# Kernel optimization log

Hardware: AMD Instinct MI355X
Metric: run time of the kernel (lower is better)

Reference implementation:

```python
import jax, jax.numpy as jnp
import numpy as np

B, S, E = 4, 2048, 512
H, D = 8, 64
MIN_W, MAX_W = 256, 1024
EPS = 1e-6


def setup_inputs() -> dict:
    key = jax.random.key(0)
    ks = jax.random.split(key, 9)
    w = lambda k, shp: jax.random.normal(k, shp, dtype=jnp.float32) * 0.02
    return {
        "x": jax.random.normal(ks[0], (B, S, E), dtype=jnp.float32),
        "rms1_w": jnp.ones((E,), jnp.float32),
        "rms2_w": jnp.ones((E,), jnp.float32),
        "qkv_w": w(ks[1], (3 * E, E)),
        "out_w": w(ks[2], (E, E)),
        "cs_w1": w(ks[3], (E // 4, E)),
        "cs_w2": w(ks[4], (1, E // 4)),
        "gate_w": w(ks[5], (2304, E)),
        "up_w": w(ks[6], (2304, E)),
        "down_w": w(ks[7], (E, 2304)),
    }


def _rmsnorm(x, w):
    rms = jax.lax.rsqrt(jnp.mean(x * x, axis=-1, keepdims=True) + EPS)
    return x * rms * w


def _rotate_half(x):
    x1 = x[..., ::2]
    x2 = x[..., 1::2]
    return jnp.stack((-x2, x1), axis=-1).reshape(x.shape)


def reference(x, rms1_w, rms2_w, qkv_w, out_w, cs_w1, cs_w2, gate_w, up_w, down_w):
    # --- pre-norm ---
    h = _rmsnorm(x, rms1_w)                                  # [B,S,E]
    # --- qkv ---
    qkv = h @ qkv_w.T                                        # [B,S,3E]
    qkv = qkv.reshape(B, S, 3, H, D).transpose(2, 0, 3, 1, 4)
    q, k, v = qkv[0], qkv[1], qkv[2]                         # [B,H,S,D]
    # --- RoPE (cat-freqs cos/sin + interleaved rotate_half, as in source) ---
    inv_freq = 1.0 / (10000.0 ** (jnp.arange(0, D, 2, dtype=jnp.float32) / D))
    pos = jnp.arange(S, dtype=jnp.float32)
    freqs = jnp.outer(pos, inv_freq)                         # [S,D/2]
    emb = jnp.concatenate([freqs, freqs], axis=-1)           # [S,D]
    cos = jnp.cos(emb)[None, None]
    sin = jnp.sin(emb)[None, None]
    q = q * cos + _rotate_half(q) * sin
    k = k * cos + _rotate_half(k) * sin
    # --- attention scores ---
    scale = D ** -0.5
    scores = jnp.einsum("bhqd,bhkd->bhqk", q, k) * scale     # [B,H,S,S]
    # --- complexity -> dynamic window size ---
    n = S * E
    mu = jnp.mean(h, axis=(1, 2), keepdims=True)
    var = jnp.sum((h - mu) ** 2, axis=(1, 2)) / (n - 1)      # unbiased, per batch
    var_norm = jax.nn.sigmoid(var * 10.0 - 5.0)
    xm = jnp.mean(h, axis=1)                                 # [B,E]
    learned = jax.nn.sigmoid((jax.nn.silu(xm @ cs_w1.T)) @ cs_w2.T)[:, 0]
    complexity = (var_norm + learned) / 2.0                  # [B]
    ws_f = MIN_W + jnp.mean(complexity) * (MAX_W - MIN_W)
    ws = ws_f.astype(jnp.int32)                              # trunc, like .int()
    ws = jnp.maximum(jnp.minimum(ws, S), MIN_W)
    # --- causal + sliding-window mask ---
    p = jnp.arange(S)
    rel = p[:, None] - p[None, :]                            # [S,S]
    allowed = (rel >= 0) & (rel < ws)
    scores = jnp.where(allowed[None, None], scores, -jnp.inf)
    attn = jax.nn.softmax(scores, axis=-1)
    out = jnp.einsum("bhqk,bhkd->bhqd", attn, v)             # [B,H,S,D]
    out = out.transpose(0, 2, 1, 3).reshape(B, S, E)
    out = out @ out_w.T
    x = x + out
    # --- SwiGLU FFN ---
    h2 = _rmsnorm(x, rms2_w)
    ffn = (jax.nn.silu(h2 @ gate_w.T) * (h2 @ up_w.T)) @ down_w.T
    return x + ffn
```

## Files before the change

kernel.cpp:

```cpp
#include <hip/hip_runtime.h>

typedef unsigned short u16;
typedef unsigned int   u32;
typedef __attribute__((ext_vector_type(4))) float  f32x4;
typedef __attribute__((ext_vector_type(8))) __bf16 bf16x8;
typedef __attribute__((ext_vector_type(4))) u32    u32x4;
typedef __attribute__((ext_vector_type(2))) u32    u32x2;

#define B_ 4
#define S_ 2048
#define E_ 512
#define H_ 8
#define D_ 64

__device__ __forceinline__ u16 f2bf(float f) {
  union { float f; u32 u; } a; a.f = f;
  u32 r = a.u + 0x7FFFu + ((a.u >> 16) & 1u);
  return (u16)(r >> 16);
}
__device__ __forceinline__ float bf2f(u16 u) {
  union { u32 u; float f; } a; a.u = (u32)u << 16;
  return a.f;
}
__device__ __forceinline__ u32 pkbf(float lo, float hi) {
  u32 r;
  asm("v_cvt_pk_bf16_f32 %0, %1, %2" : "=v"(r) : "v"(lo), "v"(hi));
  return r;
}

#define GLOAD16(gp, lp) __builtin_amdgcn_global_load_lds( \
    (const __attribute__((address_space(1))) void*)(gp),  \
    (__attribute__((address_space(3))) void*)(lp), 16, 0, 0)

__global__ __launch_bounds__(256) void cvt_k(const float* __restrict__ s,
                                             u16* __restrict__ d, int n) {
  int i = (blockIdx.x * 256 + threadIdx.x) * 4;
  if (i >= n) return;
  f32x4 v = *(const f32x4*)(s + i);
  u32x2 o;
  o.x = pkbf(v[0], v[1]);
  o.y = pkbf(v[2], v[3]);
  *(u32x2*)(d + i) = o;
}

__global__ __launch_bounds__(256) void ropetab_k(float* __restrict__ ct,
                                                 float* __restrict__ st) {
  int idx = blockIdx.x * 256 + threadIdx.x;
  int s = idx >> 6, j = idx & 63;
  float f = powf(10000.f, -(float)(j & 31) * (1.f / 32.f));
  float ang = (float)s * f;
  ct[idx] = cosf(ang);
  st[idx] = sinf(ang);
}

__global__ __launch_bounds__(256) void rmsnorm_k(const float* __restrict__ x,
                                                 const float* __restrict__ wv,
                                                 u16* __restrict__ o) {
  const int row = blockIdx.x;
  const int t = threadIdx.x;
  const float* xr = x + (size_t)row * E_;
  float v0 = xr[t], v1 = xr[t + 256];
  float ss = v0 * v0 + v1 * v1;
#pragma unroll
  for (int m = 1; m < 64; m <<= 1) ss += __shfl_xor(ss, m, 64);
  __shared__ float red[4];
  if ((t & 63) == 0) red[t >> 6] = ss;
  __syncthreads();
  float tot = red[0] + red[1] + red[2] + red[3];
  float rms = 1.f / sqrtf(tot * (1.f / (float)E_) + 1e-6f);
  o[(size_t)row * E_ + t]       = f2bf(v0 * rms * wv[t]);
  o[(size_t)row * E_ + t + 256] = f2bf(v1 * rms * wv[t + 256]);
}

__global__ __launch_bounds__(256) void colsum_k(const u16* __restrict__ h,
                                                float* __restrict__ st) {
  const int b = blockIdx.x >> 3, ck = blockIdx.x & 7;
  const u16* hb = h + ((size_t)b * S_ + ck * 256) * E_;
  const int t = threadIdx.x;
  float a0 = 0, a1 = 0, s = 0, sq = 0;
  for (int r = 0; r < 256; ++r) {
    float v0 = bf2f(hb[(size_t)r * E_ + t]);
    float v1 = bf2f(hb[(size_t)r * E_ + t + 256]);
    a0 += v0; a1 += v1;
    s += v0 + v1; sq += v0 * v0 + v1 * v1;
  }
  atomicAdd(&st[8 + b * E_ + t], a0);
  atomicAdd(&st[8 + b * E_ + t + 256], a1);
#pragma unroll
  for (int m = 1; m < 64; m <<= 1) { s += __shfl_xor(s, m, 64); sq += __shfl_xor(sq, m, 64); }
  if ((t & 63) == 0) { atomicAdd(&st[b], s); atomicAdd(&st[4 + b], sq); }
}

__global__ __launch_bounds__(128) void wscalc_k(float* __restrict__ st,
                                                const float* __restrict__ w1,
                                                const float* __restrict__ w2) {
  const int j = threadIdx.x;
  __shared__ float comp[4];
  __shared__ float tw[2];
  float dot[4] = {0.f, 0.f, 0.f, 0.f};
  const float* w1r = w1 + (size_t)j * E_;
  for (int e = 0; e < E_; ++e) {
    float wv = w1r[e];
    dot[0] += st[8 + 0 * E_ + e] * wv;
    dot[1] += st[8 + 1 * E_ + e] * wv;
    dot[2] += st[8 + 2 * E_ + e] * wv;
    dot[3] += st[8 + 3 * E_ + e] * wv;
  }
  for (int b = 0; b < 4; ++b) {
    float d = dot[b] * (1.f / (float)S_);
    float si = d / (1.f + __expf(-d));
    float term = si * w2[j];
#pragma unroll
    for (int m = 1; m < 64; m <<= 1) term += __shfl_xor(term, m, 64);
    __syncthreads();
    if ((j & 63) == 0) tw[j >> 6] = term;
    __syncthreads();
    if (j == 0) {
      float pre = tw[0] + tw[1];
      float learned = 1.f / (1.f + __expf(-pre));
      const float n = (float)S_ * (float)E_;
      float sum = st[b], ssq = st[4 + b];
      float var = (ssq - sum * sum / n) / (n - 1.f);
      float vn = 1.f / (1.f + __expf(-(var * 10.f - 5.f)));
      comp[b] = 0.5f * (vn + learned);
    }
    __syncthreads();
  }
  if (j == 0) {
    float mean = 0.25f * (comp[0] + comp[1] + comp[2] + comp[3]);
    float wsf = 256.f + mean * 768.f;
    int v = (int)wsf;
    v = v < 256 ? 256 : (v > S_ ? S_ : v);
    ((int*)st)[2056] = v;
  }
}

struct EpiArgs {
  u16* q; u16* k; u16* vt;
  const float* cosT; const float* sinT;
  const float* resid; float* outf;
};

template <int N, int K, int EPI, int WAVES>
__global__ __launch_bounds__(WAVES * 64) void gemm_k(const u16* __restrict__ A,
                                                     const u16* __restrict__ W,
                                                     EpiArgs ea) {
  __shared__ u16 sA[128 * 32];
  __shared__ u16 sB[128 * 32];
  const int tid = threadIdx.x;
  const int bm = blockIdx.x, bn = blockIdx.y;
  const int lane = tid & 63, w = tid >> 6;
  const int g = lane >> 4, c = lane & 15;
  constexpr int MI = (WAVES == 4) ? 4 : 2;
  const int wrow = (w >> 1) * ((WAVES == 4) ? 64 : 32);
  const int wcol = (w & 1) * 64;

  const int srow = tid >> 2, sch = tid & 3;
  const u16* gA = A + (size_t)(bm * 128 + srow) * K + sch * 8;
  const u16* gB = W + (size_t)(bn * 128 + srow) * K + sch * 8;
  char* lA0 = (char*)sA + w * 1024;
  char* lB0 = (char*)sB + w * 1024;

  f32x4 acc[MI][4];
  f32x4 zz = {0.f, 0.f, 0.f, 0.f};
#pragma unroll
  for (int i = 0; i < MI; ++i)
#pragma unroll
    for (int j = 0; j < 4; ++j) acc[i][j] = zz;

  for (int it = 0; it < K / 32; ++it) {
    const int ko = it * 32;
    GLOAD16(gA + ko, lA0);
    GLOAD16(gB + ko, lB0);
    if constexpr (WAVES == 4) {
      GLOAD16(gA + (size_t)64 * K + ko, lA0 + 4096);
      GLOAD16(gB + (size_t)64 * K + ko, lB0 + 4096);
    }
    __syncthreads();
    bf16x8 af[MI], bfr[4];
#pragma unroll
    for (int mi = 0; mi < MI; ++mi)
      af[mi] = *(const bf16x8*)&sA[(wrow + mi * 16 + c) * 32 + g * 8];
#pragma unroll
    for (int nj = 0; nj < 4; ++nj)
      bfr[nj] = *(const bf16x8*)&sB[(wcol + nj * 16 + c) * 32 + g * 8];
#pragma unroll
    for (int mi = 0; mi < MI; ++mi)
#pragma unroll
      for (int nj = 0; nj < 4; ++nj)
        acc[mi][nj] = __builtin_amdgcn_mfma_f32_16x16x32_bf16(af[mi], bfr[nj], acc[mi][nj], 0, 0, 0);
    __syncthreads();
  }

#pragma unroll
  for (int mi = 0; mi < MI; ++mi) {
#pragma unroll
    for (int nj = 0; nj < 4; ++nj) {
      const int rowb = bm * 128 + wrow + mi * 16 + 4 * g;
      const int cc = bn * 128 + wcol + nj * 16 + c;
      if constexpr (EPI == 0) {
        const int which = cc >> 9;
        const int hh = (cc >> 6) & 7;
        const int d = cc & 63;
        const int bi = rowb >> 11;
        const int s = rowb & (S_ - 1);
        if (which == 2) {
          u32x2 pk;
          pk.x = pkbf(acc[mi][nj][0], acc[mi][nj][1]);
          pk.y = pkbf(acc[mi][nj][2], acc[mi][nj][3]);
          *(u32x2*)(ea.vt + (((size_t)(bi * H_ + hh) * D_ + d) * S_ + s)) = pk;
        } else {
          u16* dst = (which == 0 ? ea.q : ea.k) + (((size_t)(bi * H_ + hh) * S_ + s) * D_ + d);
#pragma unroll
          for (int r = 0; r < 4; ++r) {
            float v = acc[mi][nj][r];
            float pv = __shfl_xor(v, 1, 64);
            int si = s + r;
            float cs = ea.cosT[si * 64 + d];
            float sn = ea.sinT[si * 64 + d];
            float o = v * cs + ((d & 1) ? pv : -pv) * sn;
            dst[(size_t)r * D_] = f2bf(o);
          }
        }
      } else {
#pragma unroll
        for (int r = 0; r < 4; ++r) {
          size_t idx = (size_t)(rowb + r) * N + cc;
          ea.outf[idx] = acc[mi][nj][r] + ea.resid[idx];
        }
      }
    }
  }
}

__global__ __launch_bounds__(512) void gemmgu_k(const u16* __restrict__ A,
                                                const u16* __restrict__ Wg,
                                                const u16* __restrict__ Wu,
                                                u16* __restrict__ outb) {
  __shared__ u16 sA[128 * 32];
  __shared__ u16 sG[128 * 32];
  __shared__ u16 sU[128 * 32];
  const int tid = threadIdx.x;
  const int bm = blockIdx.x, bn = blockIdx.y;
  const int lane = tid & 63, w = tid >> 6;
  const int g = lane >> 4, c = lane & 15;
  const int wrow = (w >> 1) * 32;
  const int wcol = (w & 1) * 64;

  const int srow = tid >> 2, sch = tid & 3;
  const u16* gA = A + (size_t)(bm * 128 + srow) * 512 + sch * 8;
  const u16* gG = Wg + (size_t)(bn * 128 + srow) * 512 + sch * 8;
  const u16* gU = Wu + (size_t)(bn * 128 + srow) * 512 + sch * 8;
  char* lA0 = (char*)sA + w * 1024;
  char* lG0 = (char*)sG + w * 1024;
  char* lU0 = (char*)sU + w * 1024;

  f32x4 accg[2][4], accu[2][4];
  f32x4 zz = {0.f, 0.f, 0.f, 0.f};
#pragma unroll
  for (int i = 0; i < 2; ++i)
#pragma unroll
    for (int j = 0; j < 4; ++j) { accg[i][j] = zz; accu[i][j] = zz; }

  for (int it = 0; it < 16; ++it) {
    const int ko = it * 32;
    GLOAD16(gA + ko, lA0);
    GLOAD16(gG + ko, lG0);
    GLOAD16(gU + ko, lU0);
    __syncthreads();
    bf16x8 af[2], bg[4], bu[4];
#pragma unroll
    for (int mi = 0; mi < 2; ++mi)
      af[mi] = *(const bf16x8*)&sA[(wrow + mi * 16 + c) * 32 + g * 8];
#pragma unroll
    for (int nj = 0; nj < 4; ++nj) {
      bg[nj] = *(const bf16x8*)&sG[(wcol + nj * 16 + c) * 32 + g * 8];
      bu[nj] = *(const bf16x8*)&sU[(wcol + nj * 16 + c) * 32 + g * 8];
    }
#pragma unroll
    for (int mi = 0; mi < 2; ++mi)
#pragma unroll
      for (int nj = 0; nj < 4; ++nj) {
        accg[mi][nj] = __builtin_amdgcn_mfma_f32_16x16x32_bf16(af[mi], bg[nj], accg[mi][nj], 0, 0, 0);
        accu[mi][nj] = __builtin_amdgcn_mfma_f32_16x16x32_bf16(af[mi], bu[nj], accu[mi][nj], 0, 0, 0);
      }
    __syncthreads();
  }

#pragma unroll
  for (int mi = 0; mi < 2; ++mi) {
#pragma unroll
    for (int nj = 0; nj < 4; ++nj) {
      const int rowb = bm * 128 + wrow + mi * 16 + 4 * g;
      const int cc = bn * 128 + wcol + nj * 16 + c;
#pragma unroll
      for (int r = 0; r < 4; ++r) {
        float gv = accg[mi][nj][r];
        float uv = accu[mi][nj][r];
        float sil = gv / (1.f + __expf(-gv));
        outb[(size_t)(rowb + r) * 2304 + cc] = f2bf(sil * uv);
      }
    }
  }
}

__global__ __launch_bounds__(256) void attn_k(const u16* __restrict__ Qb,
                                              const u16* __restrict__ Kb,
                                              const u16* __restrict__ Vt,
                                              u16* __restrict__ ao,
                                              const int* __restrict__ wsp) {
  const int bh = blockIdx.x;
  const int b = bh >> 3, h = bh & 7;
  const int qt = blockIdx.y;
  const int tid = threadIdx.x;
  const int w = tid >> 6, lane = tid & 63;
  const int g = lane >> 4, c = lane & 15;
  const int ws = *wsp;
  const int qw = qt * 64 + w * 16;
  const u16* Qh = Qb + (size_t)bh * S_ * D_;
  const u16* Kh = Kb + (size_t)bh * S_ * D_;
  const u16* Vh = Vt + (size_t)bh * D_ * S_;

  bf16x8 qf0 = *(const bf16x8*)(Qh + (qw + c) * D_ + g * 8);
  bf16x8 qf1 = *(const bf16x8*)(Qh + (qw + c) * D_ + 32 + g * 8);

  const float SCL = 0.125f * 1.44269504089f;
  float m2 = -3e38f, lsum = 0.f;
  f32x4 O[4];
  f32x4 zz = {0.f, 0.f, 0.f, 0.f};
#pragma unroll
  for (int i = 0; i < 4; ++i) O[i] = zz;

  int lo = qw - ws + 1;
  if (lo < 0) lo = 0;
  const int q = qw + c;
  for (int kb = lo & ~63; kb <= qw + 15; kb += 64) {
    f32x4 st[4];
#pragma unroll
    for (int t = 0; t < 4; ++t) {
      const u16* kp = Kh + (kb + 16 * t + c) * D_;
      f32x4 s = zz;
      s = __builtin_amdgcn_mfma_f32_16x16x32_bf16(*(const bf16x8*)(kp + g * 8), qf0, s, 0, 0, 0);
      s = __builtin_amdgcn_mfma_f32_16x16x32_bf16(*(const bf16x8*)(kp + 32 + g * 8), qf1, s, 0, 0, 0);
      st[t] = s;
    }
    float p[4][4];
    float bm = -3e38f;
#pragma unroll
    for (int t = 0; t < 4; ++t)
#pragma unroll
      for (int r = 0; r < 4; ++r) {
        int ki = kb + 16 * t + 4 * g + r;
        float v = st[t][r] * SCL;
        bool ok = (q >= ki) && (q - ki) < ws;
        p[t][r] = ok ? v : -__builtin_inff();
        bm = fmaxf(bm, p[t][r]);
      }
    bm = fmaxf(bm, __shfl_xor(bm, 16, 64));
    bm = fmaxf(bm, __shfl_xor(bm, 32, 64));
    if (!__all(bm - m2 <= 8.f)) {
      float mnew = fmaxf(m2, bm);
      float al = exp2f(m2 - mnew);
      lsum *= al;
#pragma unroll
      for (int i = 0; i < 4; ++i) O[i] *= al;
      m2 = mnew;
    }
    float psum = 0.f;
#pragma unroll
    for (int t = 0; t < 4; ++t)
#pragma unroll
      for (int r = 0; r < 4; ++r) {
        p[t][r] = exp2f(p[t][r] - m2);
        psum += p[t][r];
      }
    psum += __shfl_xor(psum, 16, 64);
    psum += __shfl_xor(psum, 32, 64);
    lsum += psum;

    u32 pp[4][2];
#pragma unroll
    for (int t = 0; t < 4; ++t) {
      pp[t][0] = pkbf(p[t][0], p[t][1]);
      pp[t][1] = pkbf(p[t][2], p[t][3]);
    }
    const int lA = (g & 1) * 32 + c;
    const int lB = lA + 16;
    const int hi = g >> 1;
    union { bf16x8 v; u32 u[4]; } pf0, pf1;
#pragma unroll
    for (int wi = 0; wi < 2; ++wi) {
      u32 a0 = (u32)__shfl((int)pp[0][wi], lA, 64);
      u32 a1 = (u32)__shfl((int)pp[1][wi], lA, 64);
      u32 a2 = (u32)__shfl((int)pp[2][wi], lA, 64);
      u32 a3 = (u32)__shfl((int)pp[3][wi], lA, 64);
      u32 b0 = (u32)__shfl((int)pp[0][wi], lB, 64);
      u32 b1 = (u32)__shfl((int)pp[1][wi], lB, 64);
      u32 b2 = (u32)__shfl((int)pp[2][wi], lB, 64);
      u32 b3 = (u32)__shfl((int)pp[3][wi], lB, 64);
      pf0.u[wi]     = hi ? a1 : a0;
      pf0.u[2 + wi] = hi ? b1 : b0;
      pf1.u[wi]     = hi ? a3 : a2;
      pf1.u[2 + wi] = hi ? b3 : b2;
    }
#pragma unroll
    for (int dt = 0; dt < 4; ++dt) {
      const u16* vp = Vh + (size_t)(dt * 16 + c) * S_ + kb;
      O[dt] = __builtin_amdgcn_mfma_f32_16x16x32_bf16(*(const bf16x8*)(vp + g * 8), pf0.v, O[dt], 0, 0, 0);
      O[dt] = __builtin_amdgcn_mfma_f32_16x16x32_bf16(*(const bf16x8*)(vp + 32 + g * 8), pf1.v, O[dt], 0, 0, 0);
    }
  }

  float inv = 1.f / lsum;
  __shared__ u16 ob[4][16][80];
#pragma unroll
  for (int dt = 0; dt < 4; ++dt)
#pragma unroll
    for (int r = 0; r < 4; ++r)
      ob[w][c][dt * 16 + 4 * g + r] = f2bf(O[dt][r] * inv);
  __syncthreads();
#pragma unroll
  for (int it = 0; it < 2; ++it) {
    int linear = tid + it * 256;
    int qrow = linear >> 3, ch = linear & 7;
    u32x4 v = *(const u32x4*)&ob[qrow >> 4][qrow & 15][ch * 8];
    *(u32x4*)(ao + ((size_t)(b * S_ + qt * 64 + qrow)) * E_ + h * D_ + ch * 8) = v;
  }
}

extern "C" void kernel_launch(void* const* d_in, const int* in_sizes, int n_in,
                              void* d_out, int out_size, void* d_ws, size_t ws_size,
                              hipStream_t stream) {
  const float* x      = (const float*)d_in[0];
  const float* rms1_w = (const float*)d_in[1];
  const float* rms2_w = (const float*)d_in[2];
  const float* qkv_w  = (const float*)d_in[3];
  const float* out_w  = (const float*)d_in[4];
  const float* cs_w1  = (const float*)d_in[5];
  const float* cs_w2  = (const float*)d_in[6];
  const float* gate_w = (const float*)d_in[7];
  const float* up_w   = (const float*)d_in[8];
  const float* down_w = (const float*)d_in[9];

  char* ws = (char*)d_ws;
  constexpr size_t o_wqkv = 0;
  constexpr size_t o_wout = 1572864;
  constexpr size_t o_wgate = 2097152;
  constexpr size_t o_wup = 4456448;
  constexpr size_t o_wdown = 6815744;
  constexpr size_t o_h = 9175040;
  constexpr size_t o_stats = 17563648;
  constexpr size_t o_cos = 17580032;
  constexpr size_t o_sin = 18104320;
  constexpr size_t o_Q = 18628608;
  constexpr size_t o_K = 27017216;
  constexpr size_t o_Vt = 35405824;
  constexpr size_t o_x2 = 43794432;
  constexpr size_t o_gate = 60571648;

  u16* wqkv = (u16*)(ws + o_wqkv);
  u16* wout = (u16*)(ws + o_wout);
  u16* wgate = (u16*)(ws + o_wgate);
  u16* wup = (u16*)(ws + o_wup);
  u16* wdown = (u16*)(ws + o_wdown);
  u16* h = (u16*)(ws + o_h);
  float* stats = (float*)(ws + o_stats);
  float* cosT = (float*)(ws + o_cos);
  float* sinT = (float*)(ws + o_sin);
  u16* Qb = (u16*)(ws + o_Q);
  u16* Kb = (u16*)(ws + o_K);
  u16* Vt = (u16*)(ws + o_Vt);
  float* x2 = (float*)(ws + o_x2);
  u16* gateb = (u16*)(ws + o_gate);
  u16* attno = h;
  u16* h2 = Qb;

  hipMemsetAsync(stats, 0, 16384, stream);
  cvt_k<<<768, 256, 0, stream>>>(qkv_w, wqkv, 1536 * 512);
  cvt_k<<<256, 256, 0, stream>>>(out_w, wout, 512 * 512);
  cvt_k<<<1152, 256, 0, stream>>>(gate_w, wgate, 2304 * 512);
  cvt_k<<<1152, 256, 0, stream>>>(up_w, wup, 2304 * 512);
  cvt_k<<<1152, 256, 0, stream>>>(down_w, wdown, 512 * 2304);
  ropetab_k<<<512, 256, 0, stream>>>(cosT, sinT);

  rmsnorm_k<<<8192, 256, 0, stream>>>(x, rms1_w, h);
  colsum_k<<<32, 256, 0, stream>>>(h, stats);
  wscalc_k<<<1, 128, 0, stream>>>(stats, cs_w1, cs_w2);

  EpiArgs ea{};
  ea.q = Qb; ea.k = Kb; ea.vt = Vt; ea.cosT = cosT; ea.sinT = sinT;
  gemm_k<1536, 512, 0, 4><<<dim3(64, 12), 256, 0, stream>>>(h, wqkv, ea);

  attn_k<<<dim3(32, 32), 256, 0, stream>>>(Qb, Kb, Vt, attno, (const int*)(stats + 2056));

  EpiArgs e2{};
  e2.resid = x; e2.outf = x2;
  gemm_k<512, 512, 1, 8><<<dim3(64, 4), 512, 0, stream>>>(attno, wout, e2);

  rmsnorm_k<<<8192, 256, 0, stream>>>(x2, rms2_w, h2);

  gemmgu_k<<<dim3(64, 18), 512, 0, stream>>>(h2, wgate, wup, gateb);

  EpiArgs e5{};
  e5.resid = x2; e5.outf = (float*)d_out;
  gemm_k<512, 2304, 1, 8><<<dim3(64, 4), 512, 0, stream>>>(gateb, wdown, e5);

  (void)in_sizes; (void)n_in; (void)out_size; (void)ws_size;
}
```

Baseline: 402.8 us.

## Double-buffer GEMM LDS, swizzle block order, and hoist K/V loads in attention

The GEMM kernels now use two LDS buffers, so the next K-slice is loaded while MFMAs run on the current one, which drops one barrier per iteration. Block IDs move to a flattened grid, remapped so that consecutive blocks are spread across the 8 XCDs in contiguous groups for better L2 locality. In attention, the K and V fragments are loaded early into registers and MFMA sections are wrapped in s_setprio. Tiles fully inside the window skip the mask arithmetic. The cost is doubled LDS use, which can lower occupancy, and more registers held live in attention.

```diff
diff --git a/kernel.cpp b/kernel.cpp
--- a/kernel.cpp
+++ b/kernel.cpp
@@ -145,10 +145,14 @@
 __global__ __launch_bounds__(WAVES * 64) void gemm_k(const u16* __restrict__ A,
                                                      const u16* __restrict__ W,
                                                      EpiArgs ea) {
-  __shared__ u16 sA[128 * 32];
-  __shared__ u16 sB[128 * 32];
+  constexpr int NBN = N / 128;
+  __shared__ u16 sA[2][128 * 32];
+  __shared__ u16 sB[2][128 * 32];
   const int tid = threadIdx.x;
-  const int bm = blockIdx.x, bn = blockIdx.y;
+  const int nwg = (int)gridDim.x;
+  const int bid = (int)blockIdx.x;
+  const int logical = (bid & 7) * (nwg >> 3) + (bid >> 3);
+  const int bm = logical / NBN, bn = logical % NBN;
   const int lane = tid & 63, w = tid >> 6;
   const int g = lane >> 4, c = lane & 15;
   constexpr int MI = (WAVES == 4) ? 4 : 2;
@@ -158,8 +162,7 @@
   const int srow = tid >> 2, sch = tid & 3;
   const u16* gA = A + (size_t)(bm * 128 + srow) * K + sch * 8;
   const u16* gB = W + (size_t)(bn * 128 + srow) * K + sch * 8;
-  char* lA0 = (char*)sA + w * 1024;
-  char* lB0 = (char*)sB + w * 1024;
+  const int lofs = w * 1024;
 
   f32x4 acc[MI][4];
   f32x4 zz = {0.f, 0.f, 0.f, 0.f};
@@ -168,28 +171,37 @@
 #pragma unroll
     for (int j = 0; j < 4; ++j) acc[i][j] = zz;
 
-  for (int it = 0; it < K / 32; ++it) {
-    const int ko = it * 32;
-    GLOAD16(gA + ko, lA0);
-    GLOAD16(gB + ko, lB0);
+  auto stage = [&](int buf, int ko) {
+    GLOAD16(gA + ko, (char*)sA[buf] + lofs);
+    GLOAD16(gB + ko, (char*)sB[buf] + lofs);
     if constexpr (WAVES == 4) {
-      GLOAD16(gA + (size_t)64 * K + ko, lA0 + 4096);
-      GLOAD16(gB + (size_t)64 * K + ko, lB0 + 4096);
-    }
-    __syncthreads();
+      GLOAD16(gA + (size_t)64 * K + ko, (char*)sA[buf] + lofs + 4096);
+      GLOAD16(gB + (size_t)64 * K + ko, (char*)sB[buf] + lofs + 4096);
+    }
+  };
+
+  constexpr int NIT = K / 32;
+  stage(0, 0);
+  __syncthreads();
+  int cur = 0;
+  for (int it = 0; it < NIT; ++it) {
+    if (it + 1 < NIT) stage(cur ^ 1, (it + 1) * 32);
+    const u16* bufA = sA[cur];
+    const u16* bufB = sB[cur];
     bf16x8 af[MI], bfr[4];
 #pragma unroll
     for (int mi = 0; mi < MI; ++mi)
-      af[mi] = *(const bf16x8*)&sA[(wrow + mi * 16 + c) * 32 + g * 8];
+      af[mi] = *(const bf16x8*)&bufA[(wrow + mi * 16 + c) * 32 + g * 8];
 #pragma unroll
     for (int nj = 0; nj < 4; ++nj)
-      bfr[nj] = *(const bf16x8*)&sB[(wcol + nj * 16 + c) * 32 + g * 8];
+      bfr[nj] = *(const bf16x8*)&bufB[(wcol + nj * 16 + c) * 32 + g * 8];
 #pragma unroll
     for (int mi = 0; mi < MI; ++mi)
 #pragma unroll
       for (int nj = 0; nj < 4; ++nj)
         acc[mi][nj] = __builtin_amdgcn_mfma_f32_16x16x32_bf16(af[mi], bfr[nj], acc[mi][nj], 0, 0, 0);
     __syncthreads();
+    cur ^= 1;
   }
 
 #pragma unroll
@@ -237,11 +249,14 @@
                                                 const u16* __restrict__ Wg,
                                                 const u16* __restrict__ Wu,
                                                 u16* __restrict__ outb) {
-  __shared__ u16 sA[128 * 32];
-  __shared__ u16 sG[128 * 32];
-  __shared__ u16 sU[128 * 32];
+  __shared__ u16 sA[2][128 * 32];
+  __shared__ u16 sG[2][128 * 32];
+  __shared__ u16 sU[2][128 * 32];
   const int tid = threadIdx.x;
-  const int bm = blockIdx.x, bn = blockIdx.y;
+  const int nwg = (int)gridDim.x;
+  const int bid = (int)blockIdx.x;
+  const int logical = (bid & 7) * (nwg >> 3) + (bid >> 3);
+  const int bm = logical / 18, bn = logical % 18;
   const int lane = tid & 63, w = tid >> 6;
   const int g = lane >> 4, c = lane & 15;
   const int wrow = (w >> 1) * 32;
@@ -251,9 +266,7 @@
   const u16* gA = A + (size_t)(bm * 128 + srow) * 512 + sch * 8;
   const u16* gG = Wg + (size_t)(bn * 128 + srow) * 512 + sch * 8;
   const u16* gU = Wu + (size_t)(bn * 128 + srow) * 512 + sch * 8;
-  char* lA0 = (char*)sA + w * 1024;
-  char* lG0 = (char*)sG + w * 1024;
-  char* lU0 = (char*)sU + w * 1024;
+  const int lofs = w * 1024;
 
   f32x4 accg[2][4], accu[2][4];
   f32x4 zz = {0.f, 0.f, 0.f, 0.f};
@@ -262,20 +275,28 @@
 #pragma unroll
     for (int j = 0; j < 4; ++j) { accg[i][j] = zz; accu[i][j] = zz; }
 
+  auto stage = [&](int buf, int ko) {
+    GLOAD16(gA + ko, (char*)sA[buf] + lofs);
+    GLOAD16(gG + ko, (char*)sG[buf] + lofs);
+    GLOAD16(gU + ko, (char*)sU[buf] + lofs);
+  };
+
+  stage(0, 0);
+  __syncthreads();
+  int cur = 0;
   for (int it = 0; it < 16; ++it) {
-    const int ko = it * 32;
-    GLOAD16(gA + ko, lA0);
-    GLOAD16(gG + ko, lG0);
-    GLOAD16(gU + ko, lU0);
-    __syncthreads();
+    if (it + 1 < 16) stage(cur ^ 1, (it + 1) * 32);
+    const u16* bufA = sA[cur];
+    const u16* bufG = sG[cur];
+    const u16* bufU = sU[cur];
     bf16x8 af[2], bg[4], bu[4];
 #pragma unroll
     for (int mi = 0; mi < 2; ++mi)
-      af[mi] = *(const bf16x8*)&sA[(wrow + mi * 16 + c) * 32 + g * 8];
+      af[mi] = *(const bf16x8*)&bufA[(wrow + mi * 16 + c) * 32 + g * 8];
 #pragma unroll
     for (int nj = 0; nj < 4; ++nj) {
-      bg[nj] = *(const bf16x8*)&sG[(wcol + nj * 16 + c) * 32 + g * 8];
-      bu[nj] = *(const bf16x8*)&sU[(wcol + nj * 16 + c) * 32 + g * 8];
+      bg[nj] = *(const bf16x8*)&bufG[(wcol + nj * 16 + c) * 32 + g * 8];
+      bu[nj] = *(const bf16x8*)&bufU[(wcol + nj * 16 + c) * 32 + g * 8];
     }
 #pragma unroll
     for (int mi = 0; mi < 2; ++mi)
@@ -285,6 +306,7 @@
         accu[mi][nj] = __builtin_amdgcn_mfma_f32_16x16x32_bf16(af[mi], bu[nj], accu[mi][nj], 0, 0, 0);
       }
     __syncthreads();
+    cur ^= 1;
   }
 
 #pragma unroll
@@ -335,27 +357,53 @@
   if (lo < 0) lo = 0;
   const int q = qw + c;
   for (int kb = lo & ~63; kb <= qw + 15; kb += 64) {
-    f32x4 st[4];
+    bf16x8 kf[4][2];
 #pragma unroll
     for (int t = 0; t < 4; ++t) {
       const u16* kp = Kh + (kb + 16 * t + c) * D_;
+      kf[t][0] = *(const bf16x8*)(kp + g * 8);
+      kf[t][1] = *(const bf16x8*)(kp + 32 + g * 8);
+    }
+    f32x4 st4[4];
+    __builtin_amdgcn_s_setprio(1);
+#pragma unroll
+    for (int t = 0; t < 4; ++t) {
       f32x4 s = zz;
-      s = __builtin_amdgcn_mfma_f32_16x16x32_bf16(*(const bf16x8*)(kp + g * 8), qf0, s, 0, 0, 0);
-      s = __builtin_amdgcn_mfma_f32_16x16x32_bf16(*(const bf16x8*)(kp + 32 + g * 8), qf1, s, 0, 0, 0);
-      st[t] = s;
-    }
+      s = __builtin_amdgcn_mfma_f32_16x16x32_bf16(kf[t][0], qf0, s, 0, 0, 0);
+      s = __builtin_amdgcn_mfma_f32_16x16x32_bf16(kf[t][1], qf1, s, 0, 0, 0);
+      st4[t] = s;
+    }
+    __builtin_amdgcn_s_setprio(0);
+    bf16x8 vf[4][2];
+#pragma unroll
+    for (int dt = 0; dt < 4; ++dt) {
+      const u16* vp = Vh + (size_t)(dt * 16 + c) * S_ + kb;
+      vf[dt][0] = *(const bf16x8*)(vp + g * 8);
+      vf[dt][1] = *(const bf16x8*)(vp + 32 + g * 8);
+    }
+    const bool interior = (kb + 63 <= qw) && (kb >= qw + 16 - ws);
     float p[4][4];
     float bm = -3e38f;
-#pragma unroll
-    for (int t = 0; t < 4; ++t)
-#pragma unroll
-      for (int r = 0; r < 4; ++r) {
-        int ki = kb + 16 * t + 4 * g + r;
-        float v = st[t][r] * SCL;
-        bool ok = (q >= ki) && (q - ki) < ws;
-        p[t][r] = ok ? v : -__builtin_inff();
-        bm = fmaxf(bm, p[t][r]);
-      }
+    if (interior) {
+#pragma unroll
+      for (int t = 0; t < 4; ++t)
+#pragma unroll
+        for (int r = 0; r < 4; ++r) {
+          p[t][r] = st4[t][r] * SCL;
+          bm = fmaxf(bm, p[t][r]);
+        }
+    } else {
+#pragma unroll
+      for (int t = 0; t < 4; ++t)
+#pragma unroll
+        for (int r = 0; r < 4; ++r) {
+          int ki = kb + 16 * t + 4 * g + r;
+          float v = st4[t][r] * SCL;
+          bool ok = (q >= ki) && (q - ki) < ws;
+          p[t][r] = ok ? v : -__builtin_inff();
+          bm = fmaxf(bm, p[t][r]);
+        }
+    }
     bm = fmaxf(bm, __shfl_xor(bm, 16, 64));
     bm = fmaxf(bm, __shfl_xor(bm, 32, 64));
     if (!__all(bm - m2 <= 8.f)) {
@@ -403,12 +451,13 @@
       pf1.u[wi]     = hi ? a3 : a2;
       pf1.u[2 + wi] = hi ? b3 : b2;
     }
+    __builtin_amdgcn_s_setprio(1);
 #pragma unroll
     for (int dt = 0; dt < 4; ++dt) {
-      const u16* vp = Vh + (size_t)(dt * 16 + c) * S_ + kb;
-      O[dt] = __builtin_amdgcn_mfma_f32_16x16x32_bf16(*(const bf16x8*)(vp + g * 8), pf0.v, O[dt], 0, 0, 0);
-      O[dt] = __builtin_amdgcn_mfma_f32_16x16x32_bf16(*(const bf16x8*)(vp + 32 + g * 8), pf1.v, O[dt], 0, 0, 0);
-    }
+      O[dt] = __builtin_amdgcn_mfma_f32_16x16x32_bf16(vf[dt][0], pf0.v, O[dt], 0, 0, 0);
+      O[dt] = __builtin_amdgcn_mfma_f32_16x16x32_bf16(vf[dt][1], pf1.v, O[dt], 0, 0, 0);
+    }
+    __builtin_amdgcn_s_setprio(0);
   }
 
   float inv = 1.f / lsum;
@@ -489,21 +538,21 @@
 
   EpiArgs ea{};
   ea.q = Qb; ea.k = Kb; ea.vt = Vt; ea.cosT = cosT; ea.sinT = sinT;
-  gemm_k<1536, 512, 0, 4><<<dim3(64, 12), 256, 0, stream>>>(h, wqkv, ea);
+  gemm_k<1536, 512, 0, 4><<<768, 256, 0, stream>>>(h, wqkv, ea);
 
   attn_k<<<dim3(32, 32), 256, 0, stream>>>(Qb, Kb, Vt, attno, (const int*)(stats + 2056));
 
   EpiArgs e2{};
   e2.resid = x; e2.outf = x2;
-  gemm_k<512, 512, 1, 8><<<dim3(64, 4), 512, 0, stream>>>(attno, wout, e2);
+  gemm_k<512, 512, 1, 8><<<256, 512, 0, stream>>>(attno, wout, e2);
 
   rmsnorm_k<<<8192, 256, 0, stream>>>(x2, rms2_w, h2);
 
-  gemmgu_k<<<dim3(64, 18), 512, 0, stream>>>(h2, wgate, wup, gateb);
+  gemmgu_k<<<1152, 512, 0, stream>>>(h2, wgate, wup, gateb);
 
   EpiArgs e5{};
   e5.resid = x2; e5.outf = (float*)d_out;
-  gemm_k<512, 2304, 1, 8><<<dim3(64, 4), 512, 0, stream>>>(gateb, wdown, e5);
+  gemm_k<512, 2304, 1, 8><<<256, 512, 0, stream>>>(gateb, wdown, e5);
 
   (void)in_sizes; (void)n_in; (void)out_size; (void)ws_size;
 }
```

After: 407.8 us. Within noise of the previous version (+1.2%).
